# Kernel tuning notes

Hardware: AMD Instinct MI355X
Metric: run time of the kernel (lower is better)

The kernel has to match this reference:

```python
import jax, jax.numpy as jnp
import numpy as np

SEF = 64   # skipped edge features (MLPGraphNetwork default sef)
SNF = 64   # skipped node features (MLPGraphNetwork default snf)
NR_STEPS = 3


def mlp2(x, W0, b0, W1, b1):
    # MyMLP with multI=1.0, relu hidden, linear last, no layernorm
    return jax.nn.relu(x @ W0 + b0) @ W1 + b1


def setup_inputs() -> dict:
    N, E = 50000, 800000
    nrNodeF, nrEdgeF, nrEmbed, nrTypes = 32, 3, 16, 2
    key = jax.random.key(0)
    ks = jax.random.split(key, 20)

    def w(k, fi, fo):
        # torch.normal(0,1) * (2.0 / fan_in)  (relu init in MyMLP)
        return jax.random.normal(k, (fi, fo), jnp.float32) * (2.0 / fi)

    z = lambda n: jnp.zeros((n,), jnp.float32)
    return {
        "edge_index": jax.random.randint(ks[0], (2, E), 0, N),
        "nodeFeatures": jax.random.uniform(ks[1], (N, nrNodeF), jnp.float32),
        "edgeFeatures": jax.random.normal(ks[2], (E, nrEdgeF), jnp.float32),
        "emb": jax.random.normal(ks[3], (nrTypes, nrEmbed), jnp.float32),
        "enc_n_W0": w(ks[4], nrNodeF - 1 + nrEmbed, 128), "enc_n_b0": z(128),
        "enc_n_W1": w(ks[5], 128, 128), "enc_n_b1": z(128),
        "enc_e_W0": w(ks[6], nrEdgeF, 128), "enc_e_b0": z(128),
        "enc_e_W1": w(ks[7], 128, 128), "enc_e_b1": z(128),
        "core_e_W0": w(ks[8], 192, 128), "core_e_b0": z(128),
        "core_e_W1": w(ks[9], 128, 64), "core_e_b1": z(64),
        "core_n_W0": w(ks[10], 128, 128), "core_n_b0": z(128),
        "core_n_W1": w(ks[11], 128, 64), "core_n_b1": z(64),
        "dec_W0": w(ks[12], 128, 128), "dec_b0": z(128),
        "dec_W1": w(ks[13], 128, 3), "dec_b1": z(3),
    }


def reference(edge_index, nodeFeatures, edgeFeatures, emb,
              enc_n_W0, enc_n_b0, enc_n_W1, enc_n_b1,
              enc_e_W0, enc_e_b0, enc_e_W1, enc_e_b1,
              core_e_W0, core_e_b0, core_e_W1, core_e_b1,
              core_n_W0, core_n_b0, core_n_W1, core_n_b1,
              dec_W0, dec_b0, dec_W1, dec_b1):
    N = nodeFeatures.shape[0]
    src, dst = edge_index[0], edge_index[1]  # j (source), i (target)

    # encode: embed particle type from last node feature column
    ptype = (nodeFeatures[:, -1] + 0.5).astype(jnp.int32)
    node = jnp.concatenate([nodeFeatures[:, :-1], emb[ptype]], axis=-1)
    node = mlp2(node, enc_n_W0, enc_n_b0, enc_n_W1, enc_n_b1)          # [N,128]
    edge = mlp2(edgeFeatures, enc_e_W0, enc_e_b0, enc_e_W1, enc_e_b1)  # [E,128]

    ones = jnp.ones((edge_index.shape[1],), node.dtype)
    counts = jnp.maximum(jax.ops.segment_sum(ones, dst, num_segments=N), 1.0)

    # process: shared MLPGraphNetwork applied NR_STEPS times
    for _ in range(NR_STEPS):
        einp = jnp.concatenate([edge[:, SEF:], node[dst][:, SNF:], node[src][:, SNF:]], axis=-1)  # [E,192]
        eout = mlp2(einp, core_e_W0, core_e_b0, core_e_W1, core_e_b1)  # [E,64]
        edge = jnp.concatenate([edge[:, :SEF], edge[:, SEF:] + eout], axis=-1)  # residual tail, [E,128]
        agg = jax.ops.segment_sum(edge, dst, num_segments=N) / counts[:, None]  # mean aggr, [N,128]
        ninp = jnp.concatenate([agg[:, SEF:], node[:, SNF:]], axis=-1)  # [N,128]
        nout = mlp2(ninp, core_n_W0, core_n_b0, core_n_W1, core_n_b1)  # [N,64]
        node = jnp.concatenate([node[:, :SNF], node[:, SNF:] + nout], axis=-1)  # [N,128]

    # decode
    return mlp2(node, dec_W0, dec_b0, dec_W1, dec_b1)  # [N,3]
```

## Files before the change

kernel.cpp:

```cpp
#include <hip/hip_runtime.h>
#include <cstdint>
#include <cstddef>


__global__ void k_zero(int* __restrict__ p, int n) {
    int i = blockIdx.x * 256 + threadIdx.x;
    if (i < n) p[i] = 0;
}


__global__ void k_hist(const int* __restrict__ dst, int* __restrict__ counts, int E) {
    int e = blockIdx.x * 256 + threadIdx.x;
    if (e < E) atomicAdd(&counts[dst[e]], 1);
}

__global__ __launch_bounds__(1024) void k_scan(
    const int* __restrict__ counts, int* __restrict__ row_off,
    int* __restrict__ cursor, float* __restrict__ inv_cnt, int N) {
    __shared__ int wsum[16];
    int t = threadIdx.x;
    int wave = t >> 6, lane = t & 63;
    int carry = 0;
    for (int base = 0; base < N; base += 1024) {
        int i = base + t;
        int v = (i < N) ? counts[i] : 0;
        int s = v;
        #pragma unroll
        for (int off = 1; off < 64; off <<= 1) {
            int u = __shfl_up(s, off, 64);
            if (lane >= off) s += u;
        }
        if (lane == 63) wsum[wave] = s;
        __syncthreads();
        int wpre = 0, full = 0;
        #pragma unroll
        for (int wv = 0; wv < 16; wv++) {
            int x = wsum[wv];
            full += x;
            if (wv < wave) wpre += x;
        }
        if (i < N) {
            int excl = carry + wpre + s - v;
            row_off[i] = excl;
            cursor[i]  = excl;
            inv_cnt[i] = 1.0f / (float)((v > 0) ? v : 1);
        }
        carry += full;
        __syncthreads();
    }
    if (t == 0) row_off[N] = carry;
}

__global__ void k_fill(const int* __restrict__ dst, int* __restrict__ cursor,
                       int* __restrict__ edge_list, int E) {
    int e = blockIdx.x * 256 + threadIdx.x;
    if (e < E) {
        int pos = atomicAdd(&cursor[dst[e]], 1);
        edge_list[pos] = e;
    }
}

__global__ void k_perm_idx(const int* __restrict__ elist,
                           const int* __restrict__ src, const int* __restrict__ dst,
                           int* __restrict__ src_p, int* __restrict__ dst_p, int E) {
    int i = blockIdx.x * 256 + threadIdx.x;
    if (i < E) {
        int e = elist[i];
        src_p[i] = src[e];
        dst_p[i] = dst[e];
    }
}


__global__ void k_embW(const float* __restrict__ emb, const float* __restrict__ W0,
                       const float* __restrict__ b0, float* __restrict__ embW) {
    int c = threadIdx.x;
    #pragma unroll
    for (int p = 0; p < 2; p++) {
        float acc = b0[c];
        #pragma unroll
        for (int k = 0; k < 16; k++)
            acc = fmaf(emb[p * 16 + k], W0[(31 + k) * 128 + c], acc);
        embW[p * 128 + c] = acc;
    }
}


__device__ __forceinline__ void g1_accum32(
    const float4* __restrict__ a4, int kk4,
    const float* __restrict__ W, int cbase, float* __restrict__ h) {
    #pragma clang loop unroll(disable)
    for (int kk = 0; kk < kk4; kk++) {
        float4 a = a4[kk];
        const float* wr = W + (size_t)kk * 4 * 128 + cbase;
        const float4* w0 = reinterpret_cast<const float4*>(wr);
        const float4* w1 = reinterpret_cast<const float4*>(wr + 128);
        const float4* w2 = reinterpret_cast<const float4*>(wr + 256);
        const float4* w3 = reinterpret_cast<const float4*>(wr + 384);
        #pragma unroll
        for (int cg = 0; cg < 8; cg++) {
            float4 p = w0[cg], q = w1[cg], r = w2[cg], s = w3[cg];
            h[cg*4+0] = fmaf(a.w, s.x, fmaf(a.z, r.x, fmaf(a.y, q.x, fmaf(a.x, p.x, h[cg*4+0]))));
            h[cg*4+1] = fmaf(a.w, s.y, fmaf(a.z, r.y, fmaf(a.y, q.y, fmaf(a.x, p.y, h[cg*4+1]))));
            h[cg*4+2] = fmaf(a.w, s.z, fmaf(a.z, r.z, fmaf(a.y, q.z, fmaf(a.x, p.z, h[cg*4+2]))));
            h[cg*4+3] = fmaf(a.w, s.w, fmaf(a.z, r.w, fmaf(a.y, q.w, fmaf(a.x, p.w, h[cg*4+3]))));
        }
    }
}

__device__ __forceinline__ void g1_tail3(
    float x, float y, float z, const float* __restrict__ W, int cbase,
    float* __restrict__ h) {
    const float4* w0 = reinterpret_cast<const float4*>(W + cbase);
    const float4* w1 = reinterpret_cast<const float4*>(W + 128 + cbase);
    const float4* w2 = reinterpret_cast<const float4*>(W + 256 + cbase);
    #pragma unroll
    for (int cg = 0; cg < 8; cg++) {
        float4 p = w0[cg], q = w1[cg], r = w2[cg];
        h[cg*4+0] = fmaf(z, r.x, fmaf(y, q.x, fmaf(x, p.x, h[cg*4+0])));
        h[cg*4+1] = fmaf(z, r.y, fmaf(y, q.y, fmaf(x, p.y, h[cg*4+1])));
        h[cg*4+2] = fmaf(z, r.z, fmaf(y, q.z, fmaf(x, p.z, h[cg*4+2])));
        h[cg*4+3] = fmaf(z, r.w, fmaf(y, q.w, fmaf(x, p.w, h[cg*4+3])));
    }
}

__device__ __forceinline__ void g2_accum64(
    float* __restrict__ sb, const float* __restrict__ hc,
    const float* __restrict__ W1, int kbase, int rs, float* __restrict__ o) {
    int t = threadIdx.x;
    #pragma unroll
    for (int k = 0; k < 32; k++) sb[k * 256 + t] = hc[k];
    __syncthreads();
    #pragma clang loop unroll(disable)
    for (int k = 0; k < 32; k++) {
        float hk = sb[k * 256 + t];
        const float4* w = reinterpret_cast<const float4*>(W1 + (size_t)(kbase + k) * rs);
        #pragma unroll
        for (int cg = 0; cg < 16; cg++) {
            float4 wv = w[cg];
            o[cg*4+0] = fmaf(hk, wv.x, o[cg*4+0]);
            o[cg*4+1] = fmaf(hk, wv.y, o[cg*4+1]);
            o[cg*4+2] = fmaf(hk, wv.z, o[cg*4+2]);
            o[cg*4+3] = fmaf(hk, wv.w, o[cg*4+3]);
        }
    }
    __syncthreads();
}


__global__ __launch_bounds__(256, 2) void k_enc_node_tail(
    const float* __restrict__ nodeF, const float* __restrict__ embW,
    const float* __restrict__ W0, const float* __restrict__ W1,
    const float* __restrict__ b1, float* __restrict__ nodeT, int N) {
    __shared__ float sb[32 * 256];
    int n = blockIdx.x * 256 + threadIdx.x;
    bool valid = n < N;
    int nc = valid ? n : N - 1;
    const float4* nf4 = reinterpret_cast<const float4*>(nodeF + (size_t)nc * 32);
    float4 v7 = nf4[7];
    int p = (int)(v7.w + 0.5f);
    const float4* ew = reinterpret_cast<const float4*>(embW + p * 128);

    float o[64];
    const float4* bv = reinterpret_cast<const float4*>(b1 + 64);
    #pragma unroll
    for (int i = 0; i < 16; i++) {
        float4 b = bv[i];
        o[4*i+0] = b.x; o[4*i+1] = b.y; o[4*i+2] = b.z; o[4*i+3] = b.w;
    }
    #pragma unroll
    for (int ch = 0; ch < 4; ch++) {
        int cbase = ch * 32;
        float h[32];
        #pragma unroll
        for (int i = 0; i < 8; i++) {
            float4 u = ew[ch*8 + i];
            h[4*i+0] = u.x; h[4*i+1] = u.y; h[4*i+2] = u.z; h[4*i+3] = u.w;
        }
        g1_accum32(nf4, 7, W0, cbase, h);
        g1_tail3(v7.x, v7.y, v7.z, W0 + 28*128, cbase, h);
        #pragma unroll
        for (int i = 0; i < 32; i++) h[i] = fmaxf(h[i], 0.0f);
        g2_accum64(sb, h, W1 + 64, cbase, 128, o);
    }
    if (valid) {
        float4* out4 = reinterpret_cast<float4*>(nodeT + (size_t)n * 64);
        #pragma unroll
        for (int i = 0; i < 16; i++)
            out4[i] = make_float4(o[4*i], o[4*i+1], o[4*i+2], o[4*i+3]);
    }
}


__global__ __launch_bounds__(256, 3) void k_enc_edge_T(
    const float* __restrict__ edgeF, const int* __restrict__ perm, int usePerm,
    const float* __restrict__ W0, const float* __restrict__ b0,
    const float* __restrict__ W1, const float* __restrict__ b1,
    float* __restrict__ edgeT, int E) {
    __shared__ float H[128 * 65];
    __shared__ float Wbuf[32 * 68];
    __shared__ float Xs[64 * 4];

    int t = threadIdx.x;
    int base = blockIdx.x * 64;

    if (t < 192) {
        int i = t / 3, j = t - i * 3;
        int e = base + i; int ec = (e < E) ? e : E - 1;
        int e2 = usePerm ? perm[ec] : ec;
        Xs[i * 4 + j] = edgeF[(size_t)e2 * 3 + j];
    }
    __syncthreads();

    int eg = t & 15, cg = t >> 4;
    float c1[4][8];
    {
        float4 b0a = *reinterpret_cast<const float4*>(b0 + cg * 8);
        float4 b0b = *reinterpret_cast<const float4*>(b0 + cg * 8 + 4);
        float bb[8] = {b0a.x,b0a.y,b0a.z,b0a.w,b0b.x,b0b.y,b0b.z,b0b.w};
        #pragma unroll
        for (int ie = 0; ie < 4; ie++)
            #pragma unroll
            for (int jc = 0; jc < 8; jc++) c1[ie][jc] = bb[jc];
    }
    #pragma unroll
    for (int k = 0; k < 3; k++) {
        float4 wa = *reinterpret_cast<const float4*>(W0 + k * 128 + cg * 8);
        float4 wb = *reinterpret_cast<const float4*>(W0 + k * 128 + cg * 8 + 4);
        float ww[8] = {wa.x,wa.y,wa.z,wa.w,wb.x,wb.y,wb.z,wb.w};
        #pragma unroll
        for (int ie = 0; ie < 4; ie++) {
            float a = Xs[(eg + 16 * ie) * 4 + k];
            #pragma unroll
            for (int jc = 0; jc < 8; jc++)
                c1[ie][jc] = fmaf(a, ww[jc], c1[ie][jc]);
        }
    }
    #pragma unroll
    for (int ie = 0; ie < 4; ie++)
        #pragma unroll
        for (int jc = 0; jc < 8; jc++)
            H[(cg * 8 + jc) * 65 + eg + 16 * ie] = fmaxf(c1[ie][jc], 0.0f);

    int eg2 = t & 15, cg2 = t >> 4;
    float c2[4][4];
    {
        float4 bv = *reinterpret_cast<const float4*>(b1 + 64 + cg2 * 4);
        #pragma unroll
        for (int ie = 0; ie < 4; ie++) {
            c2[ie][0]=bv.x; c2[ie][1]=bv.y; c2[ie][2]=bv.z; c2[ie][3]=bv.w;
        }
    }
    #pragma clang loop unroll(disable)
    for (int phase = 0; phase < 4; phase++) {
        __syncthreads();
        {
            int r = t >> 3, cb = t & 7;
            const float4* wr = reinterpret_cast<const float4*>(
                W1 + (size_t)(phase * 32 + r) * 128 + 64 + cb * 8);
            float* wd = Wbuf + r * 68 + cb * 8;
            float4 v0 = wr[0], v1 = wr[1];
            wd[0]=v0.x; wd[1]=v0.y; wd[2]=v0.z; wd[3]=v0.w;
            wd[4]=v1.x; wd[5]=v1.y; wd[6]=v1.z; wd[7]=v1.w;
        }
        __syncthreads();
        #pragma clang loop unroll_count(4)
        for (int k = 0; k < 32; k++) {
            int c = phase * 32 + k;
            float a0 = H[c*65 + eg2*4 + 0];
            float a1 = H[c*65 + eg2*4 + 1];
            float a2 = H[c*65 + eg2*4 + 2];
            float a3 = H[c*65 + eg2*4 + 3];
            float4 b4 = *reinterpret_cast<const float4*>(Wbuf + k * 68 + cg2 * 4);
            float bb[4] = {b4.x, b4.y, b4.z, b4.w};
            #pragma unroll
            for (int jc = 0; jc < 4; jc++) {
                c2[0][jc] = fmaf(a0, bb[jc], c2[0][jc]);
                c2[1][jc] = fmaf(a1, bb[jc], c2[1][jc]);
                c2[2][jc] = fmaf(a2, bb[jc], c2[2][jc]);
                c2[3][jc] = fmaf(a3, bb[jc], c2[3][jc]);
            }
        }
    }
    #pragma unroll
    for (int ie = 0; ie < 4; ie++) {
        int e = base + eg2 * 4 + ie;
        if (e < E) {
            *reinterpret_cast<float4*>(edgeT + (size_t)e * 64 + cg2 * 4) =
                make_float4(c2[ie][0], c2[ie][1], c2[ie][2], c2[ie][3]);
        }
    }
}


__global__ __launch_bounds__(256, 4) void k_node_pre_d(
    const float* __restrict__ nodeT, const float* __restrict__ W0,
    const float* __restrict__ b0, float* __restrict__ Pd, int N) {
    int n = blockIdx.x * 256 + threadIdx.x;
    bool valid = n < N;
    int nc = valid ? n : N - 1;
    const float4* a4 = reinterpret_cast<const float4*>(nodeT + (size_t)nc * 64);

    #pragma unroll
    for (int ch = 0; ch < 4; ch++) {
        int cbase = ch * 32;
        float h[32];
        const float4* b0v = reinterpret_cast<const float4*>(b0 + cbase);
        #pragma unroll
        for (int i = 0; i < 8; i++) {
            float4 b = b0v[i];
            h[4*i+0] = b.x; h[4*i+1] = b.y; h[4*i+2] = b.z; h[4*i+3] = b.w;
        }
        g1_accum32(a4, 16, W0 + 64*128, cbase, h);
        if (valid) {
            float4* o4 = reinterpret_cast<float4*>(Pd + (size_t)n * 128 + cbase);
            #pragma unroll
            for (int i = 0; i < 8; i++)
                o4[i] = make_float4(h[4*i], h[4*i+1], h[4*i+2], h[4*i+3]);
        }
    }
}


__global__ __launch_bounds__(256, 3) void k_edge_core_T(
    float* __restrict__ edgeT, const float* __restrict__ Pd,
    const float* __restrict__ nodeT,
    const int* __restrict__ srcI, const int* __restrict__ dstI,
    const float* __restrict__ W0, const float* __restrict__ W1,
    const float* __restrict__ b1, int E) {
    __shared__ float Abuf[2 * 64 * 65];
    __shared__ float Wbuf[32 * 132];

    int t = threadIdx.x;
    int base = blockIdx.x * 64;

    {
        int i = t >> 2, q = t & 3;
        int e = base + i; int ec = (e < E) ? e : E - 1;
        const float4* er = reinterpret_cast<const float4*>(edgeT + (size_t)ec * 64 + q * 16);
        int s = srcI[ec];
        const float4* sr = reinterpret_cast<const float4*>(nodeT + (size_t)s * 64 + q * 16);
        float* ae = Abuf + i * 65 + q * 16;
        float* as = Abuf + 64 * 65 + i * 65 + q * 16;
        #pragma unroll
        for (int j4 = 0; j4 < 4; j4++) {
            float4 v = er[j4];
            ae[j4*4+0]=v.x; ae[j4*4+1]=v.y; ae[j4*4+2]=v.z; ae[j4*4+3]=v.w;
            float4 w = sr[j4];
            as[j4*4+0]=w.x; as[j4*4+1]=w.y; as[j4*4+2]=w.z; as[j4*4+3]=w.w;
        }
    }

    int eg = t & 15, cg = t >> 4;
    float c1[4][8];
    #pragma unroll
    for (int ie = 0; ie < 4; ie++) {
        int e = base + eg + 16 * ie; int ec = (e < E) ? e : E - 1;
        int d = dstI[ec];
        const float4* pr = reinterpret_cast<const float4*>(Pd + (size_t)d * 128 + cg * 8);
        float4 p0 = pr[0], p1 = pr[1];
        c1[ie][0]=p0.x; c1[ie][1]=p0.y; c1[ie][2]=p0.z; c1[ie][3]=p0.w;
        c1[ie][4]=p1.x; c1[ie][5]=p1.y; c1[ie][6]=p1.z; c1[ie][7]=p1.w;
    }

    #pragma clang loop unroll(disable)
    for (int phase = 0; phase < 4; phase++) {
        int wrow = (phase < 2) ? phase * 32 : 128 + (phase - 2) * 32;
        const float* Asrc = Abuf + ((phase < 2) ? 0 : 64 * 65);
        int koff = (phase & 1) * 32;
        __syncthreads();
        {
            int r = t >> 3, cb = t & 7;
            const float4* wr = reinterpret_cast<const float4*>(
                W0 + (size_t)(wrow + r) * 128 + cb * 16);
            float* wd = Wbuf + r * 132 + cb * 16;
            #pragma unroll
            for (int j4 = 0; j4 < 4; j4++) {
                float4 v = wr[j4];
                wd[j4*4+0]=v.x; wd[j4*4+1]=v.y; wd[j4*4+2]=v.z; wd[j4*4+3]=v.w;
            }
        }
        __syncthreads();
        #pragma clang loop unroll_count(4)
        for (int k = 0; k < 32; k++) {
            float a0 = Asrc[(eg + 16*0)*65 + koff + k];
            float a1 = Asrc[(eg + 16*1)*65 + koff + k];
            float a2 = Asrc[(eg + 16*2)*65 + koff + k];
            float a3 = Asrc[(eg + 16*3)*65 + koff + k];
            const float* wr = Wbuf + k * 132 + cg * 8;
            float4 bq0 = *reinterpret_cast<const float4*>(wr);
            float4 bq1 = *reinterpret_cast<const float4*>(wr + 4);
            float bb[8] = {bq0.x,bq0.y,bq0.z,bq0.w,bq1.x,bq1.y,bq1.z,bq1.w};
            #pragma unroll
            for (int jc = 0; jc < 8; jc++) {
                c1[0][jc] = fmaf(a0, bb[jc], c1[0][jc]);
                c1[1][jc] = fmaf(a1, bb[jc], c1[1][jc]);
                c1[2][jc] = fmaf(a2, bb[jc], c1[2][jc]);
                c1[3][jc] = fmaf(a3, bb[jc], c1[3][jc]);
            }
        }
    }

    __syncthreads();
    float* H = Abuf;
    #pragma unroll
    for (int ie = 0; ie < 4; ie++)
        #pragma unroll
        for (int jc = 0; jc < 8; jc++)
            H[(cg*8 + jc) * 65 + eg + 16*ie] = fmaxf(c1[ie][jc], 0.0f);

    int eg2 = t & 15, cg2 = t >> 4;
    float c2[4][4];
    {
        float4 bv = *reinterpret_cast<const float4*>(b1 + cg2 * 4);
        #pragma unroll
        for (int ie = 0; ie < 4; ie++) {
            c2[ie][0]=bv.x; c2[ie][1]=bv.y; c2[ie][2]=bv.z; c2[ie][3]=bv.w;
        }
    }
    #pragma clang loop unroll(disable)
    for (int phase = 0; phase < 4; phase++) {
        __syncthreads();
        {
            int r = t >> 3, cb = t & 7;
            const float4* wr = reinterpret_cast<const float4*>(
                W1 + (size_t)(phase * 32 + r) * 64 + cb * 8);
            float* wd = Wbuf + r * 68 + cb * 8;
            float4 v0 = wr[0], v1 = wr[1];
            wd[0]=v0.x; wd[1]=v0.y; wd[2]=v0.z; wd[3]=v0.w;
            wd[4]=v1.x; wd[5]=v1.y; wd[6]=v1.z; wd[7]=v1.w;
        }
        __syncthreads();
        #pragma clang loop unroll_count(4)
        for (int k = 0; k < 32; k++) {
            int c = phase * 32 + k;
            float a0 = H[c*65 + eg2*4 + 0];
            float a1 = H[c*65 + eg2*4 + 1];
            float a2 = H[c*65 + eg2*4 + 2];
            float a3 = H[c*65 + eg2*4 + 3];
            float4 b4 = *reinterpret_cast<const float4*>(Wbuf + k * 68 + cg2 * 4);
            float bb[4] = {b4.x, b4.y, b4.z, b4.w};
            #pragma unroll
            for (int jc = 0; jc < 4; jc++) {
                c2[0][jc] = fmaf(a0, bb[jc], c2[0][jc]);
                c2[1][jc] = fmaf(a1, bb[jc], c2[1][jc]);
                c2[2][jc] = fmaf(a2, bb[jc], c2[2][jc]);
                c2[3][jc] = fmaf(a3, bb[jc], c2[3][jc]);
            }
        }
    }

    #pragma unroll
    for (int ie = 0; ie < 4; ie++) {
        int e = base + eg2 * 4 + ie;
        if (e < E) {
            float4* er = reinterpret_cast<float4*>(edgeT + (size_t)e * 64 + cg2 * 4);
            float4 old = *er;
            old.x += c2[ie][0]; old.y += c2[ie][1];
            old.z += c2[ie][2]; old.w += c2[ie][3];
            *er = old;
        }
    }
}


__global__ __launch_bounds__(256, 2) void k_edge_core_B(
    float* __restrict__ edgeT, const float* __restrict__ nodeT,
    const int* __restrict__ src, const int* __restrict__ dst,
    const float* __restrict__ W0, const float* __restrict__ b0,
    const float* __restrict__ W1, const float* __restrict__ b1, int E) {
    __shared__ float sb[32 * 256];
    int e = blockIdx.x * 256 + threadIdx.x;
    bool valid = e < E;
    int ec = valid ? e : E - 1;
    int d = dst[ec], s = src[ec];
    const float4* a4 = reinterpret_cast<const float4*>(edgeT + (size_t)ec * 64);
    const float4* d4 = reinterpret_cast<const float4*>(nodeT + (size_t)d * 64);
    const float4* s4 = reinterpret_cast<const float4*>(nodeT + (size_t)s * 64);

    float o[64];
    const float4* bv = reinterpret_cast<const float4*>(b1);
    #pragma unroll
    for (int i = 0; i < 16; i++) {
        float4 b = bv[i];
        o[4*i+0] = b.x; o[4*i+1] = b.y; o[4*i+2] = b.z; o[4*i+3] = b.w;
    }
    #pragma unroll
    for (int ch = 0; ch < 4; ch++) {
        int cbase = ch * 32;
        float h[32];
        const float4* b0v = reinterpret_cast<const float4*>(b0 + cbase);
        #pragma unroll
        for (int i = 0; i < 8; i++) {
            float4 b = b0v[i];
            h[4*i+0] = b.x; h[4*i+1] = b.y; h[4*i+2] = b.z; h[4*i+3] = b.w;
        }
        g1_accum32(a4, 16, W0, cbase, h);
        g1_accum32(d4, 16, W0 + 64*128, cbase, h);
        g1_accum32(s4, 16, W0 + 128*128, cbase, h);
        #pragma unroll
        for (int i = 0; i < 32; i++) h[i] = fmaxf(h[i], 0.0f);
        g2_accum64(sb, h, W1, cbase, 64, o);
    }
    if (valid) {
        float4* eo4 = reinterpret_cast<float4*>(edgeT + (size_t)e * 64);
        #pragma unroll
        for (int i = 0; i < 16; i++) {
            float4 t = a4[i];
            t.x += o[4*i+0]; t.y += o[4*i+1];
            t.z += o[4*i+2]; t.w += o[4*i+3];
            eo4[i] = t;
        }
    }
}


__global__ __launch_bounds__(256) void k_agg_csr(
    const float* __restrict__ edgeT, const int* __restrict__ row_off,
    const float* __restrict__ inv_cnt, float* __restrict__ aggT, int N) {
    int n = blockIdx.x * 4 + (threadIdx.x >> 6);
    int lane = threadIdx.x & 63;
    if (n >= N) return;
    int beg = row_off[n], end = row_off[n + 1];
    double s = 0.0;
    for (int idx = beg; idx < end; idx++)
        s += (double)edgeT[(size_t)idx * 64 + lane];
    aggT[(size_t)n * 64 + lane] = (float)(s * (double)inv_cnt[n]);
}

__global__ __launch_bounds__(256) void k_agg_gather(
    const float* __restrict__ edgeT, const int* __restrict__ row_off,
    const int* __restrict__ edge_list, const float* __restrict__ inv_cnt,
    float* __restrict__ aggT, int N) {
    int n = blockIdx.x * 4 + (threadIdx.x >> 6);
    int lane = threadIdx.x & 63;
    if (n >= N) return;
    int beg = row_off[n], end = row_off[n + 1];
    double s = 0.0;
    for (int idx = beg; idx < end; idx++) {
        int e = edge_list[idx];
        s += (double)edgeT[(size_t)e * 64 + lane];
    }
    aggT[(size_t)n * 64 + lane] = (float)(s * (double)inv_cnt[n]);
}


__global__ __launch_bounds__(256, 2) void k_node_core(
    const float* __restrict__ aggT, float* __restrict__ nodeT,
    const float* __restrict__ W0, const float* __restrict__ b0,
    const float* __restrict__ W1, const float* __restrict__ b1, int N) {
    __shared__ float sb[32 * 256];
    int n = blockIdx.x * 256 + threadIdx.x;
    bool valid = n < N;
    int nc = valid ? n : N - 1;
    const float4* g4 = reinterpret_cast<const float4*>(aggT + (size_t)nc * 64);
    const float4* t4 = reinterpret_cast<const float4*>(nodeT + (size_t)nc * 64);

    float o[64];
    const float4* bv = reinterpret_cast<const float4*>(b1);
    #pragma unroll
    for (int i = 0; i < 16; i++) {
        float4 b = bv[i];
        o[4*i+0] = b.x; o[4*i+1] = b.y; o[4*i+2] = b.z; o[4*i+3] = b.w;
    }
    #pragma unroll
    for (int ch = 0; ch < 4; ch++) {
        int cbase = ch * 32;
        float h[32];
        const float4* b0v = reinterpret_cast<const float4*>(b0 + cbase);
        #pragma unroll
        for (int i = 0; i < 8; i++) {
            float4 b = b0v[i];
            h[4*i+0] = b.x; h[4*i+1] = b.y; h[4*i+2] = b.z; h[4*i+3] = b.w;
        }
        g1_accum32(g4, 16, W0, cbase, h);
        g1_accum32(t4, 16, W0 + 64*128, cbase, h);
        #pragma unroll
        for (int i = 0; i < 32; i++) h[i] = fmaxf(h[i], 0.0f);
        g2_accum64(sb, h, W1, cbase, 64, o);
    }
    if (valid) {
        float4* nt4 = reinterpret_cast<float4*>(nodeT + (size_t)n * 64);
        #pragma unroll
        for (int i = 0; i < 16; i++) {
            float4 t = t4[i];
            t.x += o[4*i+0]; t.y += o[4*i+1];
            t.z += o[4*i+2]; t.w += o[4*i+3];
            nt4[i] = t;
        }
    }
}


__global__ __launch_bounds__(256, 2) void k_decode(
    const float* __restrict__ nodeF, const float* __restrict__ embW,
    const float* __restrict__ encW0, const float* __restrict__ encW1,
    const float* __restrict__ encb1, const float* __restrict__ nodeT,
    const float* __restrict__ W0, const float* __restrict__ b0,
    const float* __restrict__ W1, const float* __restrict__ b1,
    float* __restrict__ out, int N) {
    __shared__ float sb[64 * 256];
    int t = threadIdx.x;
    int n = blockIdx.x * 256 + t;
    bool valid = n < N;
    int nc = valid ? n : N - 1;
    const float4* nf4 = reinterpret_cast<const float4*>(nodeF + (size_t)nc * 32);
    const float4* t4  = reinterpret_cast<const float4*>(nodeT + (size_t)nc * 64);
    float4 v7 = nf4[7];
    int p = (int)(v7.w + 0.5f);
    const float4* ew = reinterpret_cast<const float4*>(embW + p * 128);

    float head[64];
    const float4* ebv = reinterpret_cast<const float4*>(encb1);
    #pragma unroll
    for (int i = 0; i < 16; i++) {
        float4 b = ebv[i];
        head[4*i+0] = b.x; head[4*i+1] = b.y; head[4*i+2] = b.z; head[4*i+3] = b.w;
    }
    #pragma unroll
    for (int ch = 0; ch < 4; ch++) {
        int cbase = ch * 32;
        float h[32];
        #pragma unroll
        for (int i = 0; i < 8; i++) {
            float4 u = ew[ch*8 + i];
            h[4*i+0] = u.x; h[4*i+1] = u.y; h[4*i+2] = u.z; h[4*i+3] = u.w;
        }
        g1_accum32(nf4, 7, encW0, cbase, h);
        g1_tail3(v7.x, v7.y, v7.z, encW0 + 28*128, cbase, h);
        #pragma unroll
        for (int i = 0; i < 32; i++) h[i] = fmaxf(h[i], 0.0f);
        g2_accum64(sb, h, encW1, cbase, 128, head);
    }

    #pragma unroll
    for (int k = 0; k < 64; k++) sb[k * 256 + t] = head[k];
    __syncthreads();

    float h2[128];
    #pragma unroll
    for (int ch = 0; ch < 4; ch++) {
        int cbase = ch * 32;
        float* hc = &h2[ch * 32];
        const float4* b0v = reinterpret_cast<const float4*>(b0 + cbase);
        #pragma unroll
        for (int i = 0; i < 8; i++) {
            float4 b = b0v[i];
            hc[4*i+0] = b.x; hc[4*i+1] = b.y; hc[4*i+2] = b.z; hc[4*i+3] = b.w;
        }
        #pragma clang loop unroll(disable)
        for (int k = 0; k < 64; k++) {
            float hk = sb[k * 256 + t];
            const float4* w = reinterpret_cast<const float4*>(W0 + (size_t)k * 128 + cbase);
            #pragma unroll
            for (int cg = 0; cg < 8; cg++) {
                float4 wv = w[cg];
                hc[cg*4+0] = fmaf(hk, wv.x, hc[cg*4+0]);
                hc[cg*4+1] = fmaf(hk, wv.y, hc[cg*4+1]);
                hc[cg*4+2] = fmaf(hk, wv.z, hc[cg*4+2]);
                hc[cg*4+3] = fmaf(hk, wv.w, hc[cg*4+3]);
            }
        }
        g1_accum32(t4, 16, W0 + 64*128, cbase, hc);
    }
    __syncthreads();

    float o0 = b1[0], o1 = b1[1], o2 = b1[2];
    #pragma unroll
    for (int ch = 0; ch < 4; ch++) {
        int kb = ch * 32;
        #pragma unroll
        for (int k = 0; k < 32; k++) sb[k * 256 + t] = fmaxf(h2[kb + k], 0.0f);
        __syncthreads();
        #pragma clang loop unroll(disable)
        for (int k = 0; k < 32; k++) {
            float hk = sb[k * 256 + t];
            const float* w = W1 + (size_t)(kb + k) * 3;
            o0 = fmaf(hk, w[0], o0);
            o1 = fmaf(hk, w[1], o1);
            o2 = fmaf(hk, w[2], o2);
        }
        __syncthreads();
    }
    if (valid) {
        out[(size_t)n * 3 + 0] = o0;
        out[(size_t)n * 3 + 1] = o1;
        out[(size_t)n * 3 + 2] = o2;
    }
}


extern "C" void kernel_launch(void* const* d_in, const int* in_sizes, int n_in,
                              void* d_out, int out_size, void* d_ws, size_t ws_size,
                              hipStream_t stream) {
    const int*   edge_index = (const int*)  d_in[0];
    const float* nodeF      = (const float*)d_in[1];
    const float* edgeF      = (const float*)d_in[2];
    const float* emb        = (const float*)d_in[3];
    const float* enc_n_W0   = (const float*)d_in[4];
    const float* enc_n_b0   = (const float*)d_in[5];
    const float* enc_n_W1   = (const float*)d_in[6];
    const float* enc_n_b1   = (const float*)d_in[7];
    const float* enc_e_W0   = (const float*)d_in[8];
    const float* enc_e_b0   = (const float*)d_in[9];
    const float* enc_e_W1   = (const float*)d_in[10];
    const float* enc_e_b1   = (const float*)d_in[11];
    const float* core_e_W0  = (const float*)d_in[12];
    const float* core_e_b0  = (const float*)d_in[13];
    const float* core_e_W1  = (const float*)d_in[14];
    const float* core_e_b1  = (const float*)d_in[15];
    const float* core_n_W0  = (const float*)d_in[16];
    const float* core_n_b0  = (const float*)d_in[17];
    const float* core_n_W1  = (const float*)d_in[18];
    const float* core_n_b1  = (const float*)d_in[19];
    const float* dec_W0     = (const float*)d_in[20];
    const float* dec_b0     = (const float*)d_in[21];
    const float* dec_W1     = (const float*)d_in[22];
    const float* dec_b1     = (const float*)d_in[23];
    (void)n_in; (void)out_size;

    const int E = in_sizes[0] / 2;
    const int N = in_sizes[1] / 32;
    const int* src = edge_index;
    const int* dst = edge_index + E;

    auto al = [](size_t x) { return (x + 255) & ~(size_t)255; };
    const size_t szEdgeT = al((size_t)E * 64 * 4);
    const size_t szNodeT = al((size_t)N * 64 * 4);
    const size_t szP     = al((size_t)N * 128 * 4);
    const size_t szAgg   = al((size_t)N * 64 * 4);
    const size_t szElist = al((size_t)E * 4);
    const size_t szN4    = al((size_t)N * 4);
    const size_t szRow   = al((size_t)(N + 1) * 4);
    const size_t szEmbW  = al(2 * 128 * 4);
    const size_t base = szEdgeT + szNodeT + szElist + szRow + 3 * szN4 + szEmbW;
    const size_t needCSR = base + 2 * szElist + szP;
    const size_t needAp  = base + szP;
    const int plan = (ws_size >= needCSR) ? 0 : (ws_size >= needAp) ? 1 : 2;

    char* ws = (char*)d_ws;
    size_t off = 0;
    auto carve = [&](size_t bytes) -> char* { char* p = ws + off; off += bytes; return p; };
    float* edgeT   = (float*)carve(szEdgeT);
    float* nodeT   = (float*)carve(szNodeT);
    int*   elist   = (int*)  carve(szElist);
    int*   row_off = (int*)  carve(szRow);
    int*   counts  = (int*)  carve(szN4);
    int*   cursor  = (int*)  carve(szN4);
    float* inv_cnt = (float*)carve(szN4);
    float* embW    = (float*)carve(szEmbW);
    int *src_p = nullptr, *dst_p = nullptr;
    float *Pd = nullptr, *aggT = nullptr;
    if (plan == 0) {
        src_p = (int*)carve(szElist);
        dst_p = (int*)carve(szElist);
        Pd = (float*)carve(szP); aggT = Pd;
    } else if (plan == 1) {
        Pd = (float*)carve(szP); aggT = Pd;
    } else {
        aggT = (float*)carve(szAgg);
    }

    int blkE = (E + 255) / 256;
    int blkN = (N + 255) / 256;
    int blkT = (E + 63) / 64;

    k_zero<<<(N + 255) / 256, 256, 0, stream>>>(counts, N);
    k_hist<<<blkE, 256, 0, stream>>>(dst, counts, E);
    k_scan<<<1, 1024, 0, stream>>>(counts, row_off, cursor, inv_cnt, N);
    k_fill<<<blkE, 256, 0, stream>>>(dst, cursor, elist, E);
    if (plan == 0)
        k_perm_idx<<<blkE, 256, 0, stream>>>(elist, src, dst, src_p, dst_p, E);

    k_embW<<<1, 128, 0, stream>>>(emb, enc_n_W0, enc_n_b0, embW);
    k_enc_node_tail<<<blkN, 256, 0, stream>>>(nodeF, embW, enc_n_W0, enc_n_W1,
                                              enc_n_b1, nodeT, N);
    k_enc_edge_T<<<blkT, 256, 0, stream>>>(edgeF, elist, (plan == 0) ? 1 : 0,
                                           enc_e_W0, enc_e_b0, enc_e_W1, enc_e_b1,
                                           edgeT, E);

    for (int step = 0; step < 3; step++) {
        if (plan == 0) {
            k_node_pre_d<<<blkN, 256, 0, stream>>>(nodeT, core_e_W0, core_e_b0, Pd, N);
            k_edge_core_T<<<blkT, 256, 0, stream>>>(edgeT, Pd, nodeT, src_p, dst_p,
                                                    core_e_W0, core_e_W1, core_e_b1, E);
            k_agg_csr<<<(N + 3) / 4, 256, 0, stream>>>(edgeT, row_off, inv_cnt, aggT, N);
        } else if (plan == 1) {
            k_node_pre_d<<<blkN, 256, 0, stream>>>(nodeT, core_e_W0, core_e_b0, Pd, N);
            k_edge_core_T<<<blkT, 256, 0, stream>>>(edgeT, Pd, nodeT, src, dst,
                                                    core_e_W0, core_e_W1, core_e_b1, E);
            k_agg_gather<<<(N + 3) / 4, 256, 0, stream>>>(edgeT, row_off, elist,
                                                          inv_cnt, aggT, N);
        } else {
            k_edge_core_B<<<blkE, 256, 0, stream>>>(edgeT, nodeT, src, dst,
                                                    core_e_W0, core_e_b0,
                                                    core_e_W1, core_e_b1, E);
            k_agg_gather<<<(N + 3) / 4, 256, 0, stream>>>(edgeT, row_off, elist,
                                                          inv_cnt, aggT, N);
        }
        k_node_core<<<blkN, 256, 0, stream>>>(aggT, nodeT, core_n_W0, core_n_b0,
                                              core_n_W1, core_n_b1, N);
    }
    k_decode<<<blkN, 256, 0, stream>>>(nodeF, embW, enc_n_W0, enc_n_W1, enc_n_b1,
                                       nodeT, dec_W0, dec_b0, dec_W1, dec_b1,
                                       (float*)d_out, N);
}
```

Baseline: 3.063 ms.

## Prefetch weight tiles into registers and retile node-core MLP via shared memory

The edge encoder and edge core kernels now load the next weight tile from global memory into registers while the current tile is being consumed from shared memory. This hides global-load latency behind the FMA loop instead of stalling between the two barriers. The per-thread-per-node node-core kernel is replaced by a 64-node block-tiled version that stages inputs and weights in shared memory with the same register prefetch. That removes the large per-thread register arrays and raises weight reuse, at the cost of extra shared memory and more barriers.

Result: faster. 2.859 ms (-6.7%).

```diff
diff --git a/kernel.cpp b/kernel.cpp
--- a/kernel.cpp
+++ b/kernel.cpp
@@ -236,6 +236,15 @@
                 c1[ie][jc] = fmaf(a, ww[jc], c1[ie][jc]);
         }
     }
+
+    int wr_r = t >> 3, wr_cb = t & 7;
+    float4 wreg2[2];
+    {
+        const float4* wr = reinterpret_cast<const float4*>(
+            W1 + (size_t)(wr_r) * 128 + 64 + wr_cb * 8);
+        wreg2[0] = wr[0]; wreg2[1] = wr[1];
+    }
+
     #pragma unroll
     for (int ie = 0; ie < 4; ie++)
         #pragma unroll
@@ -255,15 +264,16 @@
     for (int phase = 0; phase < 4; phase++) {
         __syncthreads();
         {
-            int r = t >> 3, cb = t & 7;
+            float* wd = Wbuf + wr_r * 68 + wr_cb * 8;
+            wd[0]=wreg2[0].x; wd[1]=wreg2[0].y; wd[2]=wreg2[0].z; wd[3]=wreg2[0].w;
+            wd[4]=wreg2[1].x; wd[5]=wreg2[1].y; wd[6]=wreg2[1].z; wd[7]=wreg2[1].w;
+        }
+        __syncthreads();
+        if (phase < 3) {
             const float4* wr = reinterpret_cast<const float4*>(
-                W1 + (size_t)(phase * 32 + r) * 128 + 64 + cb * 8);
-            float* wd = Wbuf + r * 68 + cb * 8;
-            float4 v0 = wr[0], v1 = wr[1];
-            wd[0]=v0.x; wd[1]=v0.y; wd[2]=v0.z; wd[3]=v0.w;
-            wd[4]=v1.x; wd[5]=v1.y; wd[6]=v1.z; wd[7]=v1.w;
-        }
-        __syncthreads();
+                W1 + (size_t)((phase + 1) * 32 + wr_r) * 128 + 64 + wr_cb * 8);
+            wreg2[0] = wr[0]; wreg2[1] = wr[1];
+        }
         #pragma clang loop unroll_count(4)
         for (int k = 0; k < 32; k++) {
             int c = phase * 32 + k;
@@ -363,33 +373,42 @@
         c1[ie][4]=p1.x; c1[ie][5]=p1.y; c1[ie][6]=p1.z; c1[ie][7]=p1.w;
     }
 
+    int wr_r = t >> 3, wr_cb = t & 7;
+    float4 wreg[4];
+    {
+        const float4* wr = reinterpret_cast<const float4*>(
+            W0 + (size_t)(0 + wr_r) * 128 + wr_cb * 16);
+        wreg[0]=wr[0]; wreg[1]=wr[1]; wreg[2]=wr[2]; wreg[3]=wr[3];
+    }
     #pragma clang loop unroll(disable)
     for (int phase = 0; phase < 4; phase++) {
-        int wrow = (phase < 2) ? phase * 32 : 128 + (phase - 2) * 32;
         const float* Asrc = Abuf + ((phase < 2) ? 0 : 64 * 65);
         int koff = (phase & 1) * 32;
         __syncthreads();
         {
-            int r = t >> 3, cb = t & 7;
+            float* wd = Wbuf + wr_r * 132 + wr_cb * 16;
+            #pragma unroll
+            for (int j4 = 0; j4 < 4; j4++) {
+                wd[j4*4+0]=wreg[j4].x; wd[j4*4+1]=wreg[j4].y;
+                wd[j4*4+2]=wreg[j4].z; wd[j4*4+3]=wreg[j4].w;
+            }
+        }
+        __syncthreads();
+        if (phase < 3) {
+            int wrow_n = (phase + 1 < 2) ? (phase + 1) * 32 : 128 + (phase - 1) * 32;
             const float4* wr = reinterpret_cast<const float4*>(
-                W0 + (size_t)(wrow + r) * 128 + cb * 16);
-            float* wd = Wbuf + r * 132 + cb * 16;
-            #pragma unroll
-            for (int j4 = 0; j4 < 4; j4++) {
-                float4 v = wr[j4];
-                wd[j4*4+0]=v.x; wd[j4*4+1]=v.y; wd[j4*4+2]=v.z; wd[j4*4+3]=v.w;
-            }
-        }
-        __syncthreads();
+                W0 + (size_t)(wrow_n + wr_r) * 128 + wr_cb * 16);
+            wreg[0]=wr[0]; wreg[1]=wr[1]; wreg[2]=wr[2]; wreg[3]=wr[3];
+        }
         #pragma clang loop unroll_count(4)
         for (int k = 0; k < 32; k++) {
             float a0 = Asrc[(eg + 16*0)*65 + koff + k];
             float a1 = Asrc[(eg + 16*1)*65 + koff + k];
             float a2 = Asrc[(eg + 16*2)*65 + koff + k];
             float a3 = Asrc[(eg + 16*3)*65 + koff + k];
-            const float* wr = Wbuf + k * 132 + cg * 8;
-            float4 bq0 = *reinterpret_cast<const float4*>(wr);
-            float4 bq1 = *reinterpret_cast<const float4*>(wr + 4);
+            const float* wrp = Wbuf + k * 132 + cg * 8;
+            float4 bq0 = *reinterpret_cast<const float4*>(wrp);
+            float4 bq1 = *reinterpret_cast<const float4*>(wrp + 4);
             float bb[8] = {bq0.x,bq0.y,bq0.z,bq0.w,bq1.x,bq1.y,bq1.z,bq1.w};
             #pragma unroll
             for (int jc = 0; jc < 8; jc++) {
@@ -401,6 +420,13 @@
         }
     }
 
+    float4 wreg2[2];
+    {
+        const float4* wr = reinterpret_cast<const float4*>(
+            W1 + (size_t)(wr_r) * 64 + wr_cb * 8);
+        wreg2[0] = wr[0]; wreg2[1] = wr[1];
+    }
+
     __syncthreads();
     float* H = Abuf;
     #pragma unroll
@@ -422,15 +448,16 @@
     for (int phase = 0; phase < 4; phase++) {
         __syncthreads();
         {
-            int r = t >> 3, cb = t & 7;
+            float* wd = Wbuf + wr_r * 68 + wr_cb * 8;
+            wd[0]=wreg2[0].x; wd[1]=wreg2[0].y; wd[2]=wreg2[0].z; wd[3]=wreg2[0].w;
+            wd[4]=wreg2[1].x; wd[5]=wreg2[1].y; wd[6]=wreg2[1].z; wd[7]=wreg2[1].w;
+        }
+        __syncthreads();
+        if (phase < 3) {
             const float4* wr = reinterpret_cast<const float4*>(
-                W1 + (size_t)(phase * 32 + r) * 64 + cb * 8);
-            float* wd = Wbuf + r * 68 + cb * 8;
-            float4 v0 = wr[0], v1 = wr[1];
-            wd[0]=v0.x; wd[1]=v0.y; wd[2]=v0.z; wd[3]=v0.w;
-            wd[4]=v1.x; wd[5]=v1.y; wd[6]=v1.z; wd[7]=v1.w;
-        }
-        __syncthreads();
+                W1 + (size_t)((phase + 1) * 32 + wr_r) * 64 + wr_cb * 8);
+            wreg2[0] = wr[0]; wreg2[1] = wr[1];
+        }
         #pragma clang loop unroll_count(4)
         for (int k = 0; k < 32; k++) {
             int c = phase * 32 + k;
@@ -459,6 +486,160 @@
             old.x += c2[ie][0]; old.y += c2[ie][1];
             old.z += c2[ie][2]; old.w += c2[ie][3];
             *er = old;
+        }
+    }
+}
+
+
+__global__ __launch_bounds__(256, 3) void k_node_core_T(
+    const float* __restrict__ aggT, float* __restrict__ nodeT,
+    const float* __restrict__ W0, const float* __restrict__ b0,
+    const float* __restrict__ W1, const float* __restrict__ b1, int N) {
+    __shared__ float Abuf[64 * 132];
+    __shared__ float Wbuf[32 * 132];
+
+    int t = threadIdx.x;
+    int base = blockIdx.x * 64;
+
+    {
+        int i = t >> 2, q = t & 3;
+        int n = base + i; int nc = (n < N) ? n : N - 1;
+        const float4* gr = reinterpret_cast<const float4*>(aggT + (size_t)nc * 64 + q * 16);
+        const float4* tr = reinterpret_cast<const float4*>(nodeT + (size_t)nc * 64 + q * 16);
+        float* ag = Abuf + i * 132 + q * 16;
+        float* at = Abuf + i * 132 + 64 + q * 16;
+        #pragma unroll
+        for (int j4 = 0; j4 < 4; j4++) {
+            float4 v = gr[j4];
+            ag[j4*4+0]=v.x; ag[j4*4+1]=v.y; ag[j4*4+2]=v.z; ag[j4*4+3]=v.w;
+            float4 w = tr[j4];
+            at[j4*4+0]=w.x; at[j4*4+1]=w.y; at[j4*4+2]=w.z; at[j4*4+3]=w.w;
+        }
+    }
+
+    int ng = t & 15, cg = t >> 4;
+    float c1[4][8];
+    {
+        float4 b0a = *reinterpret_cast<const float4*>(b0 + cg * 8);
+        float4 b0b = *reinterpret_cast<const float4*>(b0 + cg * 8 + 4);
+        float bb[8] = {b0a.x,b0a.y,b0a.z,b0a.w,b0b.x,b0b.y,b0b.z,b0b.w};
+        #pragma unroll
+        for (int in = 0; in < 4; in++)
+            #pragma unroll
+            for (int jc = 0; jc < 8; jc++) c1[in][jc] = bb[jc];
+    }
+
+    int wr_r = t >> 3, wr_cb = t & 7;
+    float4 wreg[4];
+    {
+        const float4* wr = reinterpret_cast<const float4*>(
+            W0 + (size_t)(wr_r) * 128 + wr_cb * 16);
+        wreg[0]=wr[0]; wreg[1]=wr[1]; wreg[2]=wr[2]; wreg[3]=wr[3];
+    }
+    #pragma clang loop unroll(disable)
+    for (int phase = 0; phase < 4; phase++) {
+        int koff = phase * 32;
+        __syncthreads();
+        {
+            float* wd = Wbuf + wr_r * 132 + wr_cb * 16;
+            #pragma unroll
+            for (int j4 = 0; j4 < 4; j4++) {
+                wd[j4*4+0]=wreg[j4].x; wd[j4*4+1]=wreg[j4].y;
+                wd[j4*4+2]=wreg[j4].z; wd[j4*4+3]=wreg[j4].w;
+            }
+        }
+        __syncthreads();
+        if (phase < 3) {
+            const float4* wr = reinterpret_cast<const float4*>(
+                W0 + (size_t)((phase + 1) * 32 + wr_r) * 128 + wr_cb * 16);
+            wreg[0]=wr[0]; wreg[1]=wr[1]; wreg[2]=wr[2]; wreg[3]=wr[3];
+        }
+        #pragma clang loop unroll_count(4)
+        for (int k = 0; k < 32; k++) {
+            float a0 = Abuf[(ng + 16*0)*132 + koff + k];
+            float a1 = Abuf[(ng + 16*1)*132 + koff + k];
+            float a2 = Abuf[(ng + 16*2)*132 + koff + k];
+            float a3 = Abuf[(ng + 16*3)*132 + koff + k];
+            const float* wrp = Wbuf + k * 132 + cg * 8;
+            float4 bq0 = *reinterpret_cast<const float4*>(wrp);
+            float4 bq1 = *reinterpret_cast<const float4*>(wrp + 4);
+            float bb[8] = {bq0.x,bq0.y,bq0.z,bq0.w,bq1.x,bq1.y,bq1.z,bq1.w};
+            #pragma unroll
+            for (int jc = 0; jc < 8; jc++) {
+                c1[0][jc] = fmaf(a0, bb[jc], c1[0][jc]);
+                c1[1][jc] = fmaf(a1, bb[jc], c1[1][jc]);
+                c1[2][jc] = fmaf(a2, bb[jc], c1[2][jc]);
+                c1[3][jc] = fmaf(a3, bb[jc], c1[3][jc]);
+            }
+        }
+    }
+
+    float4 wreg2[2];
+    {
+        const float4* wr = reinterpret_cast<const float4*>(
+            W1 + (size_t)(wr_r) * 64 + wr_cb * 8);
+        wreg2[0] = wr[0]; wreg2[1] = wr[1];
+    }
+
+    __syncthreads();
+    float* H = Abuf;
+    #pragma unroll
+    for (int in = 0; in < 4; in++)
+        #pragma unroll
+        for (int jc = 0; jc < 8; jc++)
+            H[(cg*8 + jc) * 65 + ng + 16*in] = fmaxf(c1[in][jc], 0.0f);
+
+    int ng2 = t & 15, cg2 = t >> 4;
+    float c2[4][4];
+    {
+        float4 bv = *reinterpret_cast<const float4*>(b1 + cg2 * 4);
+        #pragma unroll
+        for (int in = 0; in < 4; in++) {
+            c2[in][0]=bv.x; c2[in][1]=bv.y; c2[in][2]=bv.z; c2[in][3]=bv.w;
+        }
+    }
+    #pragma clang loop unroll(disable)
+    for (int phase = 0; phase < 4; phase++) {
+        __syncthreads();
+        {
+            float* wd = Wbuf + wr_r * 68 + wr_cb * 8;
+            wd[0]=wreg2[0].x; wd[1]=wreg2[0].y; wd[2]=wreg2[0].z; wd[3]=wreg2[0].w;
+            wd[4]=wreg2[1].x; wd[5]=wreg2[1].y; wd[6]=wreg2[1].z; wd[7]=wreg2[1].w;
+        }
+        __syncthreads();
+        if (phase < 3) {
+            const float4* wr = reinterpret_cast<const float4*>(
+                W1 + (size_t)((phase + 1) * 32 + wr_r) * 64 + wr_cb * 8);
+            wreg2[0] = wr[0]; wreg2[1] = wr[1];
+        }
+        #pragma clang loop unroll_count(4)
+        for (int k = 0; k < 32; k++) {
+            int c = phase * 32 + k;
+            float a0 = H[c*65 + ng2*4 + 0];
+            float a1 = H[c*65 + ng2*4 + 1];
+            float a2 = H[c*65 + ng2*4 + 2];
+            float a3 = H[c*65 + ng2*4 + 3];
+            float4 b4 = *reinterpret_cast<const float4*>(Wbuf + k * 68 + cg2 * 4);
+            float bb[4] = {b4.x, b4.y, b4.z, b4.w};
+            #pragma unroll
+            for (int jc = 0; jc < 4; jc++) {
+                c2[0][jc] = fmaf(a0, bb[jc], c2[0][jc]);
+                c2[1][jc] = fmaf(a1, bb[jc], c2[1][jc]);
+                c2[2][jc] = fmaf(a2, bb[jc], c2[2][jc]);
+                c2[3][jc] = fmaf(a3, bb[jc], c2[3][jc]);
+            }
+        }
+    }
+
+    #pragma unroll
+    for (int in = 0; in < 4; in++) {
+        int n = base + ng2 * 4 + in;
+        if (n < N) {
+            float4* nr = reinterpret_cast<float4*>(nodeT + (size_t)n * 64 + cg2 * 4);
+            float4 old = *nr;
+            old.x += c2[in][0]; old.y += c2[in][1];
+            old.z += c2[in][2]; old.w += c2[in][3];
+            *nr = old;
         }
     }
 }
@@ -542,53 +723,6 @@
         s += (double)edgeT[(size_t)e * 64 + lane];
     }
     aggT[(size_t)n * 64 + lane] = (float)(s * (double)inv_cnt[n]);
-}
-
-
-__global__ __launch_bounds__(256, 2) void k_node_core(
-    const float* __restrict__ aggT, float* __restrict__ nodeT,
-    const float* __restrict__ W0, const float* __restrict__ b0,
-    const float* __restrict__ W1, const float* __restrict__ b1, int N) {
-    __shared__ float sb[32 * 256];
-    int n = blockIdx.x * 256 + threadIdx.x;
-    bool valid = n < N;
-    int nc = valid ? n : N - 1;
-    const float4* g4 = reinterpret_cast<const float4*>(aggT + (size_t)nc * 64);
-    const float4* t4 = reinterpret_cast<const float4*>(nodeT + (size_t)nc * 64);
-
-    float o[64];
-    const float4* bv = reinterpret_cast<const float4*>(b1);
-    #pragma unroll
-    for (int i = 0; i < 16; i++) {
-        float4 b = bv[i];
-        o[4*i+0] = b.x; o[4*i+1] = b.y; o[4*i+2] = b.z; o[4*i+3] = b.w;
-    }
-    #pragma unroll
-    for (int ch = 0; ch < 4; ch++) {
-        int cbase = ch * 32;
-        float h[32];
-        const float4* b0v = reinterpret_cast<const float4*>(b0 + cbase);
-        #pragma unroll
-        for (int i = 0; i < 8; i++) {
-            float4 b = b0v[i];
-            h[4*i+0] = b.x; h[4*i+1] = b.y; h[4*i+2] = b.z; h[4*i+3] = b.w;
-        }
-        g1_accum32(g4, 16, W0, cbase, h);
-        g1_accum32(t4, 16, W0 + 64*128, cbase, h);
-        #pragma unroll
-        for (int i = 0; i < 32; i++) h[i] = fmaxf(h[i], 0.0f);
-        g2_accum64(sb, h, W1, cbase, 64, o);
-    }
-    if (valid) {
-        float4* nt4 = reinterpret_cast<float4*>(nodeT + (size_t)n * 64);
-        #pragma unroll
-        for (int i = 0; i < 16; i++) {
-            float4 t = t4[i];
-            t.x += o[4*i+0]; t.y += o[4*i+1];
-            t.z += o[4*i+2]; t.w += o[4*i+3];
-            nt4[i] = t;
-        }
-    }
 }
 
 
@@ -764,6 +898,7 @@
     int blkE = (E + 255) / 256;
     int blkN = (N + 255) / 256;
     int blkT = (E + 63) / 64;
+    int blkNT = (N + 63) / 64;
 
     k_zero<<<(N + 255) / 256, 256, 0, stream>>>(counts, N);
     k_hist<<<blkE, 256, 0, stream>>>(dst, counts, E);
@@ -798,8 +933,8 @@
             k_agg_gather<<<(N + 3) / 4, 256, 0, stream>>>(edgeT, row_off, elist,
                                                           inv_cnt, aggT, N);
         }
-        k_node_core<<<blkN, 256, 0, stream>>>(aggT, nodeT, core_n_W0, core_n_b0,
-                                              core_n_W1, core_n_b1, N);
+        k_node_core_T<<<blkNT, 256, 0, stream>>>(aggT, nodeT, core_n_W0, core_n_b0,
+                                                 core_n_W1, core_n_b1, N);
     }
     k_decode<<<blkN, 256, 0, stream>>>(nodeF, embW, enc_n_W0, enc_n_W1, enc_n_b1,
                                        nodeT, dec_W0, dec_b0, dec_W1, dec_b1,
```
